# Performance work log

Hardware: AMD Instinct MI355X
Metric: run time of the kernel (lower is better)

## Reference

```python
import jax, jax.numpy as jnp
import numpy as np

IB = 8      # input/hidden activation bits
ABMVM = 8   # gate activation bits after MVM
ABNM = 8    # near-memory compute bits
NL = 0.05   # analog noise level
CY_DIV = 2.0
CY_SCALE = 2.0


def quant_pass(x, wb, sign):
    # Faithful port of QuantFunc.forward: clip/clamp then fake-quant (round to grid).
    if wb is None or wb == 0:
        return x
    if sign:
        delta = 0.0 if wb == 1 else 1.0 / (2.0 ** (wb - 1))
        x = jnp.clip(x, -1.0 + delta, 1.0 - delta)
    else:
        x = jnp.clip(x, 0.0, 1.0)
    if wb == 1:
        return jnp.sign(x)
    scale = 2.0 ** (wb - 1) if sign else 2.0 ** wb
    return jnp.round(x * scale) / scale


def setup_inputs() -> dict:
    key = jax.random.key(0)
    ks = jax.random.split(key, 7)
    B, I, H = 4096, 1024, 1024
    return {
        "input": jax.random.normal(ks[0], (B, I), jnp.float32),
        "hx": jax.random.normal(ks[1], (B, H), jnp.float32),
        "cx": jax.random.normal(ks[2], (B, H), jnp.float32),
        "weight_ih": jax.random.normal(ks[3], (4 * H, I), jnp.float32) * 0.1,
        "weight_hh": jax.random.normal(ks[4], (4 * H, H), jnp.float32) * 0.1,
        "bias_ih": jax.random.normal(ks[5], (4 * H,), jnp.float32) * 0.1,
        "bias_hh": jax.random.normal(ks[6], (4 * H,), jnp.float32) * 0.1,
        "train": 0,
    }


def reference(input, hx, cx, weight_ih, weight_hh, bias_ih, bias_hh, train):
    # Per-call Gaussian noise (simulated analog hardware); fixed key for reproducibility.
    nk = jax.random.split(jax.random.key(42), 4)
    noise_w_ih = jax.random.normal(nk[0], weight_ih.T.shape, weight_ih.dtype) * weight_ih.max() * NL
    noise_w_hh = jax.random.normal(nk[1], weight_hh.T.shape, weight_hh.dtype) * weight_hh.max() * NL
    noise_b_ih = jax.random.normal(nk[2], bias_ih.shape, bias_ih.dtype) * bias_ih.max() * NL
    noise_b_hh = jax.random.normal(nk[3], bias_hh.shape, bias_hh.dtype) * bias_hh.max() * NL

    # gates: [B, 4H]
    gates = (quant_pass(input, IB, True) @ (weight_ih.T + noise_w_ih) + bias_ih + noise_b_ih
             + quant_pass(hx, IB, True) @ (weight_hh.T + noise_w_hh) + bias_hh + noise_b_hh)

    ingate, forgetgate, cellgate, outgate = jnp.split(gates, 4, axis=1)
    ingate = quant_pass(jax.nn.sigmoid(ingate), ABMVM, False)
    forgetgate = quant_pass(jax.nn.sigmoid(forgetgate), ABMVM, False)
    cellgate = quant_pass(jnp.tanh(cellgate), ABMVM, True)
    outgate = quant_pass(jax.nn.sigmoid(outgate), ABMVM, False)

    cy = quant_pass((quant_pass(forgetgate * cx, ABNM, True)
                     + quant_pass(ingate * cellgate, ABNM, True)) / CY_DIV, ABNM, True)
    hy = quant_pass(outgate * quant_pass(jnp.tanh(cy * CY_SCALE), ABNM, True), ABNM, True)
    return (hy, cy)
```

## Files before the change

kernel.cpp:

```cpp
#include <hip/hip_runtime.h>
#include <hip/hip_bf16.h>
#include <stdint.h>
#include <stddef.h>


#define PART 1

typedef __attribute__((ext_vector_type(8))) short bf16x8;
typedef __attribute__((ext_vector_type(4))) float f32x4;

#define BATCH 4096

#define WS_A_OFF    ((size_t)0)
#define WS_B_OFF    ((size_t)16 << 20)
#define WS_BIAS_OFF ((size_t)48 << 20)
#define WS_MAX_OFF  (WS_BIAS_OFF + 16384)

__host__ __device__ inline void tf2x32(uint32_t k0, uint32_t k1,
                                       uint32_t x0, uint32_t x1,
                                       uint32_t &o0, uint32_t &o1)
{
  const uint32_t k2 = k0 ^ k1 ^ 0x1BD11BDAu;
#define TFR(r) { x0 += x1; x1 = (x1 << (r)) | (x1 >> (32 - (r))); x1 ^= x0; }
  x0 += k0; x1 += k1;
  TFR(13) TFR(15) TFR(26) TFR(6)
  x0 += k1; x1 += k2 + 1u;
  TFR(17) TFR(29) TFR(16) TFR(24)
  x0 += k2; x1 += k0 + 2u;
  TFR(13) TFR(15) TFR(26) TFR(6)
  x0 += k0; x1 += k1 + 3u;
  TFR(17) TFR(29) TFR(16) TFR(24)
  x0 += k1; x1 += k2 + 4u;
  TFR(13) TFR(15) TFR(26) TFR(6)
  x0 += k2; x1 += k0 + 5u;
#undef TFR
  o0 = x0; o1 = x1;
}

__device__ inline uint32_t jax_bits32(uint32_t k0, uint32_t k1, uint32_t i, uint32_t size)
{
#if PART
  uint32_t a, b;
  tf2x32(k0, k1, 0u, i, a, b);
  return a ^ b;
#else
  uint32_t half = size >> 1, a, b;
  if (i < half) { tf2x32(k0, k1, i, i + half, a, b); return a; }
  tf2x32(k0, k1, i - half, i, a, b); return b;
#endif
}

__device__ inline float bits_to_normal(uint32_t bits)
{
  float f = __uint_as_float((bits >> 9) | 0x3F800000u) - 1.0f;
  const float lo = -0x1.fffffep-1f;
  float u = fmaxf(lo, f * 2.0f + lo);
  float w = -log1pf(-u * u);
  float p;
  if (w < 5.0f) {
    w -= 2.5f;
    p = 2.81022636e-08f;
    p = fmaf(p, w, 3.43273939e-07f);
    p = fmaf(p, w, -3.5233877e-06f);
    p = fmaf(p, w, -4.39150654e-06f);
    p = fmaf(p, w, 0.00021858087f);
    p = fmaf(p, w, -0.00125372503f);
    p = fmaf(p, w, -0.00417768164f);
    p = fmaf(p, w, 0.246640727f);
    p = fmaf(p, w, 1.50140941f);
  } else {
    w = sqrtf(w) - 3.0f;
    p = -0.000200214257f;
    p = fmaf(p, w, 0.000100950558f);
    p = fmaf(p, w, 0.00134934322f);
    p = fmaf(p, w, -0.00367342844f);
    p = fmaf(p, w, 0.00573950773f);
    p = fmaf(p, w, -0.0076224613f);
    p = fmaf(p, w, 0.00943887047f);
    p = fmaf(p, w, 1.00167406f);
    p = fmaf(p, w, 2.83297682f);
  }
  return 0x1.6a09e6p+0f * (p * u);
}

__device__ inline float quantS8(float x)
{
  x = fminf(fmaxf(x, -0.9921875f), 0.9921875f);
  return rintf(x * 128.0f) * 0.0078125f;
}
__device__ inline float quantU8(float x)
{
  x = fminf(fmaxf(x, 0.0f), 1.0f);
  return rintf(x * 256.0f) * 0.00390625f;
}
__device__ inline float sigmoid_xla(float x) { return 0.5f + 0.5f * tanhf(0.5f * x); }

__device__ inline unsigned short f2bf(float x)
{
  uint32_t b = __float_as_uint(x);
  return (unsigned short)((b + 0x7FFFu + ((b >> 16) & 1u)) >> 16);
}
__device__ inline float bf2f(unsigned short u) { return __uint_as_float(((uint32_t)u) << 16); }

__device__ inline float dec_max(uint32_t u)
{
  uint32_t bits = (u & 0x80000000u) ? (u ^ 0x80000000u) : ~u;
  return __uint_as_float(bits);
}

__global__ void init_max(uint32_t* mx)
{
  if (threadIdx.x < 4) mx[threadIdx.x] = 0u;
}

__global__ void kmax(const float4* __restrict__ a, int n4, uint32_t* __restrict__ out)
{
  float m = -3.4e38f;
  for (int i = blockIdx.x * blockDim.x + threadIdx.x; i < n4; i += gridDim.x * blockDim.x) {
    float4 v = a[i];
    m = fmaxf(fmaxf(m, fmaxf(v.x, v.y)), fmaxf(v.z, v.w));
  }
  for (int off = 32; off; off >>= 1) m = fmaxf(m, __shfl_down(m, off, 64));
  __shared__ float sm[4];
  if ((threadIdx.x & 63) == 0) sm[threadIdx.x >> 6] = m;
  __syncthreads();
  if (threadIdx.x == 0) {
    float bm = sm[0];
    for (int w = 1; w < (int)(blockDim.x >> 6); ++w) bm = fmaxf(bm, sm[w]);
    uint32_t bits = __float_as_uint(bm);
    uint32_t enc = (bits & 0x80000000u) ? ~bits : (bits | 0x80000000u);
    atomicMax(out, enc);
  }
}

__global__ void build_A(const float4* __restrict__ in, const float4* __restrict__ hx,
                        unsigned short* __restrict__ A)
{
  int t = blockIdx.x * 256 + threadIdx.x;
  int b = t >> 9;
  int kq = t & 511;
  float4 v = (kq < 256) ? in[b * 256 + kq] : hx[b * 256 + (kq - 256)];
  unsigned short o[4];
  o[0] = f2bf(quantS8(v.x)); o[1] = f2bf(quantS8(v.y));
  o[2] = f2bf(quantS8(v.z)); o[3] = f2bf(quantS8(v.w));
  *reinterpret_cast<uint64_t*>(A + (size_t)t * 4) = *reinterpret_cast<uint64_t*>(o);
}

__global__ void build_B(const float* __restrict__ wih, const float* __restrict__ whh,
                        unsigned short* __restrict__ B, const uint32_t* __restrict__ mxenc,
                        uint32_t kih0, uint32_t kih1, uint32_t khh0, uint32_t khh1)
{
  uint32_t t = blockIdx.x * 256u + threadIdx.x;
  uint32_t arr = t >> 22;
  uint32_t r = t & 4194303u;
  uint32_t k = r & 1023u;
  uint32_t n = r >> 10;
  const float* w = arr ? whh : wih;
  float mx = dec_max(mxenc[arr]);
  uint32_t key0 = arr ? khh0 : kih0, key1 = arr ? khh1 : kih1;
  uint32_t i = k * 4096u + n;
  float nrm = bits_to_normal(jax_bits32(key0, key1, i, 4194304u));
  float weff = w[(size_t)n * 1024u + k] + (nrm * mx) * 0.05f;
  unsigned short hi = f2bf(weff);
  unsigned short lob = f2bf(weff - bf2f(hi));
  uint32_t np = (n & 1023u) * 4u + (n >> 10);
  size_t base = (size_t)np * 4096u + (arr ? 1024u : 0u) + k;
  B[base] = hi;
  B[base + 2048u] = lob;
}

__global__ void build_bias(const float* __restrict__ bih, const float* __restrict__ bhh,
                           float* __restrict__ biasE, const uint32_t* __restrict__ mxenc,
                           uint32_t kbi0, uint32_t kbi1, uint32_t kbh0, uint32_t kbh1)
{
  uint32_t j = blockIdx.x * 256u + threadIdx.x;
  if (j >= 4096u) return;
  float mi = dec_max(mxenc[2]), mh = dec_max(mxenc[3]);
  float ni = (bits_to_normal(jax_bits32(kbi0, kbi1, j, 4096u)) * mi) * 0.05f;
  float nh = (bits_to_normal(jax_bits32(kbh0, kbh1, j, 4096u)) * mh) * 0.05f;
  biasE[(j & 1023u) * 4u + (j >> 10)] = ((bih[j] + ni) + bhh[j]) + nh;
}

__device__ __forceinline__ void gload_lds16(const void* g, void* l)
{
  __builtin_amdgcn_global_load_lds((__attribute__((address_space(1))) void*)g,
                                   (__attribute__((address_space(3))) void*)l, 16, 0, 0);
}

#define VM4  asm volatile("s_waitcnt vmcnt(4)" ::: "memory")
#define VM0  asm volatile("s_waitcnt vmcnt(0)" ::: "memory")
#define NOVM

#define TILE_ONE(t_, DO_STAGE_, VM_ASM_)                                          \
  {                                                                               \
    const int buf_ = (t_) & 3;                                                    \
    const unsigned char* pa_ = lds + buf_ * 32768 + aoff;                         \
    const unsigned char* pb_ = lds + buf_ * 32768 + boff;                         \
    bf16x8 bfr_[4], afL_[4], afH_[4];                                             \
    _Pragma("unroll") for (int n_ = 0; n_ < 4; ++n_)                              \
      bfr_[n_] = *(const bf16x8*)(pb_ + n_ * 1024);                               \
    _Pragma("unroll") for (int m_ = 0; m_ < 4; ++m_)                              \
      afL_[m_] = *(const bf16x8*)(pa_ + m_ * 1024);                               \
    _Pragma("unroll") for (int m_ = 0; m_ < 4; ++m_)                              \
      afH_[m_] = *(const bf16x8*)(pa_ + (4 + m_) * 1024);                         \
    if (DO_STAGE_) {                                                              \
      const int ts_ = (t_) + 2;                                                   \
      unsigned char* la_ = lds + (ts_ & 3) * 32768;                               \
      const int ka_ = (ts_ * 32) & 2047;                                          \
      const size_t kb_ = (size_t)ts_ * 32;                                        \
      gload_lds16(Ar0 + ka_, la_ + tid * 16);                                     \
      gload_lds16(Ar1 + ka_, la_ + 8192 + tid * 16);                              \
      gload_lds16(Br0 + kb_, la_ + 16384 + tid * 16);                             \
      gload_lds16(Br1 + kb_, la_ + 16384 + 8192 + tid * 16);                      \
    }                                                                             \
    __builtin_amdgcn_s_setprio(1);                                                \
    _Pragma("unroll") for (int m_ = 0; m_ < 4; ++m_)                              \
      _Pragma("unroll") for (int n_ = 0; n_ < 4; ++n_)                            \
        acc[m_][n_] = __builtin_amdgcn_mfma_f32_16x16x32_bf16(afL_[m_], bfr_[n_], \
                                                              acc[m_][n_], 0, 0, 0); \
    _Pragma("unroll") for (int m_ = 0; m_ < 4; ++m_)                              \
      _Pragma("unroll") for (int n_ = 0; n_ < 4; ++n_)                            \
        acc[4 + m_][n_] = __builtin_amdgcn_mfma_f32_16x16x32_bf16(afH_[m_], bfr_[n_], \
                                                              acc[4 + m_][n_], 0, 0, 0); \
    __builtin_amdgcn_s_setprio(0);                                                \
    VM_ASM_;                                                                      \
    __builtin_amdgcn_s_barrier();                                                 \
    __builtin_amdgcn_sched_barrier(0);                                            \
  }

__global__ __launch_bounds__(512, 2) void gemm_gates(
    const unsigned short* __restrict__ A,
    const unsigned short* __restrict__ B,
    const float* __restrict__ bias,
    const float* __restrict__ cx,
    float* __restrict__ hy,
    float* __restrict__ cy)
{
  extern __shared__ unsigned char lds[];
  const int tid  = threadIdx.x;
  const int lane = tid & 63;
  const int wave = tid >> 6;
  const int wr = wave >> 2;
  const int wc = wave & 3;

  const int bid = blockIdx.x;
  const int wg  = (bid & 7) * 32 + (bid >> 3);
  const int brow = (wg & 15) * 256;
  const int bcol = (wg >> 4) * 256;

  int sr0, sk0, sr1, sk1;
  {
    int c = tid, p = c >> 3, lc = (c & 7) ^ (p & 7);
    sr0 = p * 2 + (lc >> 2); sk0 = (lc & 3) * 8;
    c = tid + 512; p = c >> 3; lc = (c & 7) ^ (p & 7);
    sr1 = p * 2 + (lc >> 2); sk1 = (lc & 3) * 8;
  }
  const unsigned short* Ar0 = A + (size_t)(brow + sr0) * 2048 + sk0;
  const unsigned short* Ar1 = A + (size_t)(brow + sr1) * 2048 + sk1;
  const unsigned short* Br0 = B + (size_t)(bcol + sr0) * 4096 + sk0;
  const unsigned short* Br1 = B + (size_t)(bcol + sr1) * 4096 + sk1;

  const int lrh = (lane & 15) >> 1;
  const int chk = ((((lane & 1) << 2) | (lane >> 4)) ^ lrh);
  const int aoff = wr * 8192 + lrh * 128 + chk * 16;
  const int boff = 16384 + wc * 4096 + lrh * 128 + chk * 16;

  f32x4 acc[8][4] = {};

#pragma unroll
  for (int tt = 0; tt < 2; ++tt) {
    unsigned char* la = lds + tt * 32768;
    const int ka = tt * 32;
    gload_lds16(Ar0 + ka, la + tid * 16);
    gload_lds16(Ar1 + ka, la + 8192 + tid * 16);
    gload_lds16(Br0 + (size_t)(tt * 32), la + 16384 + tid * 16);
    gload_lds16(Br1 + (size_t)(tt * 32), la + 16384 + 8192 + tid * 16);
  }
  VM4;
  __builtin_amdgcn_s_barrier();
  __builtin_amdgcn_sched_barrier(0);

#pragma unroll 1
  for (int t = 0; t < 126; ++t) {
    TILE_ONE(t, 1, VM4);
  }
  TILE_ONE(126, 0, VM0);
  TILE_ONE(127, 0, NOVM);

  float* LT = (float*)lds;
  const int col_local0 = wc * 64 + (lane & 15);
  const int lrow = (lane >> 4) << 2;
  const int h = tid & 63;
  const int hg = (bcol >> 2) + h;

#pragma unroll
  for (int hh = 0; hh < 2; ++hh) {
    __syncthreads();
#pragma unroll
    for (int m = 0; m < 4; ++m) {
#pragma unroll
      for (int n = 0; n < 4; ++n) {
        const int cl = col_local0 + n * 16;
        const float bv = bias[bcol + cl];
        const int lr0 = wr * 64 + m * 16 + lrow;
#pragma unroll
        for (int r = 0; r < 4; ++r)
          LT[(lr0 + r) * 256 + cl] = acc[hh * 4 + m][n][r] + bv;
      }
    }
    __syncthreads();
#pragma unroll
    for (int i = 0; i < 16; ++i) {
      const int lr = (tid >> 6) * 16 + i;
      const int grow = brow + ((lr >> 6) << 7) + hh * 64 + (lr & 63);
      const float4 q = *(const float4*)(LT + lr * 256 + 4 * h);
      const size_t oidx = (size_t)grow * 1024 + hg;
      float ing = quantU8(sigmoid_xla(q.x));
      float fg  = quantU8(sigmoid_xla(q.y));
      float cg  = quantS8(tanhf(q.z));
      float og  = quantU8(sigmoid_xla(q.w));
      float c0  = cx[oidx];
      float cyv = quantS8((quantS8(fg * c0) + quantS8(ing * cg)) * 0.5f);
      float hyv = quantS8(og * quantS8(tanhf(cyv * 2.0f)));
      hy[oidx] = hyv;
      cy[oidx] = cyv;
    }
  }
}

extern "C" void kernel_launch(void* const* d_in, const int* in_sizes, int n_in,
                              void* d_out, int out_size, void* d_ws, size_t ws_size,
                              hipStream_t stream)
{
  const float* input = (const float*)d_in[0];
  const float* hx    = (const float*)d_in[1];
  const float* cx    = (const float*)d_in[2];
  const float* wih   = (const float*)d_in[3];
  const float* whh   = (const float*)d_in[4];
  const float* bih   = (const float*)d_in[5];
  const float* bhh   = (const float*)d_in[6];
  (void)in_sizes; (void)n_in; (void)ws_size;

  uint8_t* ws = (uint8_t*)d_ws;
  unsigned short* A   = (unsigned short*)(ws + WS_A_OFF);
  unsigned short* B   = (unsigned short*)(ws + WS_B_OFF);
  float* biasE        = (float*)(ws + WS_BIAS_OFF);
  uint32_t* mx        = (uint32_t*)(ws + WS_MAX_OFF);

  uint32_t nk[4][2];
#if PART
  for (int i = 0; i < 4; ++i) tf2x32(0u, 42u, 0u, (uint32_t)i, nk[i][0], nk[i][1]);
#else
  {
    uint32_t w0[4], w1[4];
    for (int i = 0; i < 4; ++i) tf2x32(0u, 42u, (uint32_t)i, (uint32_t)(i + 4), w0[i], w1[i]);
    uint32_t out8[8] = {w0[0], w0[1], w0[2], w0[3], w1[0], w1[1], w1[2], w1[3]};
    for (int i = 0; i < 4; ++i) { nk[i][0] = out8[2 * i]; nk[i][1] = out8[2 * i + 1]; }
  }
#endif

  init_max<<<1, 64, 0, stream>>>(mx);
  kmax<<<1024, 256, 0, stream>>>((const float4*)wih, 1048576, mx + 0);
  kmax<<<1024, 256, 0, stream>>>((const float4*)whh, 1048576, mx + 1);
  kmax<<<4, 256, 0, stream>>>((const float4*)bih, 1024, mx + 2);
  kmax<<<4, 256, 0, stream>>>((const float4*)bhh, 1024, mx + 3);

  build_A<<<8192, 256, 0, stream>>>((const float4*)input, (const float4*)hx, A);
  build_B<<<32768, 256, 0, stream>>>(wih, whh, B, mx, nk[0][0], nk[0][1], nk[1][0], nk[1][1]);
  build_bias<<<16, 256, 0, stream>>>(bih, bhh, biasE, mx, nk[2][0], nk[2][1], nk[3][0], nk[3][1]);

  float* hy = (float*)d_out;
  float* cyp = hy + (size_t)BATCH * 1024;

  (void)hipFuncSetAttribute((const void*)gemm_gates,
                            hipFuncAttributeMaxDynamicSharedMemorySize, 131072);
  gemm_gates<<<dim3(256), dim3(512), 131072, stream>>>(A, B, biasE, cx, hy, cyp);
}
```

Baseline: 230.6 us.

## Fuse prep kernels, split-bf16 B with double buffering, pad epilogue LDS tile

Merges the four max-reduction launches into one kernel and the A/B/bias build kernels into one, cutting launch count. The GEMM main loop is restructured to stage both hi and lo bf16 halves of B in a double-buffered 48KB LDS layout. Each K-tile is now 64 tiles with extra barriers between MFMA phases, and it waits with vmcnt(0) each iteration instead of the old 4-deep ring. The epilogue LDS transpose stride is padded to 272 floats to reduce bank conflicts. The shallower prefetch and added barriers risk exposing memory latency, and the LDS footprint rises.

```diff
diff --git a/kernel.cpp b/kernel.cpp
--- a/kernel.cpp
+++ b/kernel.cpp
@@ -113,11 +113,20 @@
   if (threadIdx.x < 4) mx[threadIdx.x] = 0u;
 }
 
-__global__ void kmax(const float4* __restrict__ a, int n4, uint32_t* __restrict__ out)
-{
+__global__ void kmax_all(const float4* __restrict__ wih, const float4* __restrict__ whh,
+                         const float4* __restrict__ bih, const float4* __restrict__ bhh,
+                         uint32_t* __restrict__ mx)
+{
+  const int blk = blockIdx.x;
+  const float4* src; int n4, bl, nb; uint32_t* out;
+  if (blk < 1024)      { src = wih; n4 = 1048576; bl = blk;        nb = 1024; out = mx + 0; }
+  else if (blk < 2048) { src = whh; n4 = 1048576; bl = blk - 1024; nb = 1024; out = mx + 1; }
+  else if (blk < 2052) { src = bih; n4 = 1024;    bl = blk - 2048; nb = 4;    out = mx + 2; }
+  else                 { src = bhh; n4 = 1024;    bl = blk - 2052; nb = 4;    out = mx + 3; }
+
   float m = -3.4e38f;
-  for (int i = blockIdx.x * blockDim.x + threadIdx.x; i < n4; i += gridDim.x * blockDim.x) {
-    float4 v = a[i];
+  for (int i = bl * 256 + threadIdx.x; i < n4; i += nb * 256) {
+    float4 v = src[i];
     m = fmaxf(fmaxf(m, fmaxf(v.x, v.y)), fmaxf(v.z, v.w));
   }
   for (int off = 32; off; off >>= 1) m = fmaxf(m, __shfl_down(m, off, 64));
@@ -125,60 +134,56 @@
   if ((threadIdx.x & 63) == 0) sm[threadIdx.x >> 6] = m;
   __syncthreads();
   if (threadIdx.x == 0) {
-    float bm = sm[0];
-    for (int w = 1; w < (int)(blockDim.x >> 6); ++w) bm = fmaxf(bm, sm[w]);
+    float bm = fmaxf(fmaxf(sm[0], sm[1]), fmaxf(sm[2], sm[3]));
     uint32_t bits = __float_as_uint(bm);
     uint32_t enc = (bits & 0x80000000u) ? ~bits : (bits | 0x80000000u);
     atomicMax(out, enc);
   }
 }
 
-__global__ void build_A(const float4* __restrict__ in, const float4* __restrict__ hx,
-                        unsigned short* __restrict__ A)
-{
-  int t = blockIdx.x * 256 + threadIdx.x;
-  int b = t >> 9;
-  int kq = t & 511;
-  float4 v = (kq < 256) ? in[b * 256 + kq] : hx[b * 256 + (kq - 256)];
-  unsigned short o[4];
-  o[0] = f2bf(quantS8(v.x)); o[1] = f2bf(quantS8(v.y));
-  o[2] = f2bf(quantS8(v.z)); o[3] = f2bf(quantS8(v.w));
-  *reinterpret_cast<uint64_t*>(A + (size_t)t * 4) = *reinterpret_cast<uint64_t*>(o);
-}
-
-__global__ void build_B(const float* __restrict__ wih, const float* __restrict__ whh,
-                        unsigned short* __restrict__ B, const uint32_t* __restrict__ mxenc,
-                        uint32_t kih0, uint32_t kih1, uint32_t khh0, uint32_t khh1)
-{
-  uint32_t t = blockIdx.x * 256u + threadIdx.x;
-  uint32_t arr = t >> 22;
-  uint32_t r = t & 4194303u;
-  uint32_t k = r & 1023u;
-  uint32_t n = r >> 10;
-  const float* w = arr ? whh : wih;
-  float mx = dec_max(mxenc[arr]);
-  uint32_t key0 = arr ? khh0 : kih0, key1 = arr ? khh1 : kih1;
-  uint32_t i = k * 4096u + n;
-  float nrm = bits_to_normal(jax_bits32(key0, key1, i, 4194304u));
-  float weff = w[(size_t)n * 1024u + k] + (nrm * mx) * 0.05f;
-  unsigned short hi = f2bf(weff);
-  unsigned short lob = f2bf(weff - bf2f(hi));
-  uint32_t np = (n & 1023u) * 4u + (n >> 10);
-  size_t base = (size_t)np * 4096u + (arr ? 1024u : 0u) + k;
-  B[base] = hi;
-  B[base + 2048u] = lob;
-}
-
-__global__ void build_bias(const float* __restrict__ bih, const float* __restrict__ bhh,
-                           float* __restrict__ biasE, const uint32_t* __restrict__ mxenc,
-                           uint32_t kbi0, uint32_t kbi1, uint32_t kbh0, uint32_t kbh1)
-{
-  uint32_t j = blockIdx.x * 256u + threadIdx.x;
-  if (j >= 4096u) return;
-  float mi = dec_max(mxenc[2]), mh = dec_max(mxenc[3]);
-  float ni = (bits_to_normal(jax_bits32(kbi0, kbi1, j, 4096u)) * mi) * 0.05f;
-  float nh = (bits_to_normal(jax_bits32(kbh0, kbh1, j, 4096u)) * mh) * 0.05f;
-  biasE[(j & 1023u) * 4u + (j >> 10)] = ((bih[j] + ni) + bhh[j]) + nh;
+__global__ void build_all(const float* __restrict__ wih, const float* __restrict__ whh,
+                          const float4* __restrict__ in, const float4* __restrict__ hxp,
+                          const float* __restrict__ bih, const float* __restrict__ bhh,
+                          unsigned short* __restrict__ A, unsigned short* __restrict__ B,
+                          float* __restrict__ biasE, const uint32_t* __restrict__ mxenc,
+                          uint32_t kih0, uint32_t kih1, uint32_t khh0, uint32_t khh1,
+                          uint32_t kbi0, uint32_t kbi1, uint32_t kbh0, uint32_t kbh1)
+{
+  const uint32_t blk = blockIdx.x;
+  if (blk < 32768u) {
+    uint32_t t = blk * 256u + threadIdx.x;
+    uint32_t arr = t >> 22;
+    uint32_t r = t & 4194303u;
+    uint32_t k = r & 1023u;
+    uint32_t n = r >> 10;
+    const float* w = arr ? whh : wih;
+    float mx = dec_max(mxenc[arr]);
+    uint32_t key0 = arr ? khh0 : kih0, key1 = arr ? khh1 : kih1;
+    uint32_t i = k * 4096u + n;
+    float nrm = bits_to_normal(jax_bits32(key0, key1, i, 4194304u));
+    float weff = w[(size_t)n * 1024u + k] + (nrm * mx) * 0.05f;
+    unsigned short hi = f2bf(weff);
+    unsigned short lob = f2bf(weff - bf2f(hi));
+    uint32_t np = (n & 1023u) * 4u + (n >> 10);
+    size_t base = (size_t)np * 4096u + (arr ? 1024u : 0u) + k;
+    B[base] = hi;
+    B[base + 2048u] = lob;
+  } else if (blk < 40960u) {
+    int t = (int)(blk - 32768u) * 256 + threadIdx.x;
+    int b = t >> 9;
+    int kq = t & 511;
+    float4 v = (kq < 256) ? in[b * 256 + kq] : hxp[b * 256 + (kq - 256)];
+    unsigned short o[4];
+    o[0] = f2bf(quantS8(v.x)); o[1] = f2bf(quantS8(v.y));
+    o[2] = f2bf(quantS8(v.z)); o[3] = f2bf(quantS8(v.w));
+    *reinterpret_cast<uint64_t*>(A + (size_t)t * 4) = *reinterpret_cast<uint64_t*>(o);
+  } else {
+    uint32_t j = (blk - 40960u) * 256u + threadIdx.x;
+    float mi = dec_max(mxenc[2]), mh = dec_max(mxenc[3]);
+    float ni = (bits_to_normal(jax_bits32(kbi0, kbi1, j, 4096u)) * mi) * 0.05f;
+    float nh = (bits_to_normal(jax_bits32(kbh0, kbh1, j, 4096u)) * mh) * 0.05f;
+    biasE[(j & 1023u) * 4u + (j >> 10)] = ((bih[j] + ni) + bhh[j]) + nh;
+  }
 }
 
 __device__ __forceinline__ void gload_lds16(const void* g, void* l)
@@ -187,46 +192,74 @@
                                    (__attribute__((address_space(3))) void*)l, 16, 0, 0);
 }
 
-#define VM4  asm volatile("s_waitcnt vmcnt(4)" ::: "memory")
 #define VM0  asm volatile("s_waitcnt vmcnt(0)" ::: "memory")
 #define NOVM
+#define SBAR __builtin_amdgcn_s_barrier()
+#define SCB  __builtin_amdgcn_sched_barrier(0)
+
+#define BUFSZ 49152
 
 #define TILE_ONE(t_, DO_STAGE_, VM_ASM_)                                          \
   {                                                                               \
-    const int buf_ = (t_) & 3;                                                    \
-    const unsigned char* pa_ = lds + buf_ * 32768 + aoff;                         \
-    const unsigned char* pb_ = lds + buf_ * 32768 + boff;                         \
-    bf16x8 bfr_[4], afL_[4], afH_[4];                                             \
+    const int buf_ = (t_) & 1;                                                    \
+    const unsigned char* pa_  = lds + buf_ * BUFSZ + aoff;                        \
+    const unsigned char* pbh_ = lds + buf_ * BUFSZ + 16384 + boffU;               \
+    const unsigned char* pbl_ = lds + buf_ * BUFSZ + 32768 + boffU;               \
+    bf16x8 bh_[4], bl_[4], afL_[4], afH_[4];                                      \
+                 \
     _Pragma("unroll") for (int n_ = 0; n_ < 4; ++n_)                              \
-      bfr_[n_] = *(const bf16x8*)(pb_ + n_ * 1024);                               \
+      bh_[n_] = *(const bf16x8*)(pbh_ + n_ * 1024);                               \
     _Pragma("unroll") for (int m_ = 0; m_ < 4; ++m_)                              \
       afL_[m_] = *(const bf16x8*)(pa_ + m_ * 1024);                               \
-    _Pragma("unroll") for (int m_ = 0; m_ < 4; ++m_)                              \
-      afH_[m_] = *(const bf16x8*)(pa_ + (4 + m_) * 1024);                         \
     if (DO_STAGE_) {                                                              \
-      const int ts_ = (t_) + 2;                                                   \
-      unsigned char* la_ = lds + (ts_ & 3) * 32768;                               \
-      const int ka_ = (ts_ * 32) & 2047;                                          \
-      const size_t kb_ = (size_t)ts_ * 32;                                        \
+      const int ts_ = (t_) + 1;                                                   \
+      unsigned char* la_ = lds + (ts_ & 1) * BUFSZ;                               \
+      const int ka_ = ts_ * 32;                                                   \
       gload_lds16(Ar0 + ka_, la_ + tid * 16);                                     \
       gload_lds16(Ar1 + ka_, la_ + 8192 + tid * 16);                              \
-      gload_lds16(Br0 + kb_, la_ + 16384 + tid * 16);                             \
-      gload_lds16(Br1 + kb_, la_ + 16384 + 8192 + tid * 16);                      \
+      gload_lds16(Br0 + ka_, la_ + 16384 + tid * 16);                             \
+      gload_lds16(Br1 + ka_, la_ + 16384 + 8192 + tid * 16);                      \
+      gload_lds16(Br0 + 2048 + ka_, la_ + 32768 + tid * 16);                      \
+      gload_lds16(Br1 + 2048 + ka_, la_ + 32768 + 8192 + tid * 16);               \
     }                                                                             \
+    SBAR; SCB;                                                                    \
     __builtin_amdgcn_s_setprio(1);                                                \
     _Pragma("unroll") for (int m_ = 0; m_ < 4; ++m_)                              \
       _Pragma("unroll") for (int n_ = 0; n_ < 4; ++n_)                            \
-        acc[m_][n_] = __builtin_amdgcn_mfma_f32_16x16x32_bf16(afL_[m_], bfr_[n_], \
+        acc[m_][n_] = __builtin_amdgcn_mfma_f32_16x16x32_bf16(afL_[m_], bh_[n_],  \
                                                               acc[m_][n_], 0, 0, 0); \
+    __builtin_amdgcn_s_setprio(0);                                                \
+    SBAR; SCB;                                                                    \
+                                                       \
+    _Pragma("unroll") for (int m_ = 0; m_ < 4; ++m_)                              \
+      afH_[m_] = *(const bf16x8*)(pa_ + (4 + m_) * 1024);                         \
+    SBAR; SCB;                                                                    \
+    __builtin_amdgcn_s_setprio(1);                                                \
     _Pragma("unroll") for (int m_ = 0; m_ < 4; ++m_)                              \
       _Pragma("unroll") for (int n_ = 0; n_ < 4; ++n_)                            \
-        acc[4 + m_][n_] = __builtin_amdgcn_mfma_f32_16x16x32_bf16(afH_[m_], bfr_[n_], \
+        acc[4 + m_][n_] = __builtin_amdgcn_mfma_f32_16x16x32_bf16(afH_[m_], bh_[n_], \
+                                                              acc[4 + m_][n_], 0, 0, 0); \
+    __builtin_amdgcn_s_setprio(0);                                                \
+    SBAR; SCB;                                                                    \
+                         \
+    _Pragma("unroll") for (int n_ = 0; n_ < 4; ++n_)                              \
+      bl_[n_] = *(const bf16x8*)(pbl_ + n_ * 1024);                               \
+    SBAR; SCB;                                                                    \
+    __builtin_amdgcn_s_setprio(1);                                                \
+    _Pragma("unroll") for (int m_ = 0; m_ < 4; ++m_)                              \
+      _Pragma("unroll") for (int n_ = 0; n_ < 4; ++n_)                            \
+        acc[m_][n_] = __builtin_amdgcn_mfma_f32_16x16x32_bf16(afL_[m_], bl_[n_],  \
+                                                              acc[m_][n_], 0, 0, 0); \
+    _Pragma("unroll") for (int m_ = 0; m_ < 4; ++m_)                              \
+      _Pragma("unroll") for (int n_ = 0; n_ < 4; ++n_)                            \
+        acc[4 + m_][n_] = __builtin_amdgcn_mfma_f32_16x16x32_bf16(afH_[m_], bl_[n_], \
                                                               acc[4 + m_][n_], 0, 0, 0); \
     __builtin_amdgcn_s_setprio(0);                                                \
     VM_ASM_;                                                                      \
-    __builtin_amdgcn_s_barrier();                                                 \
-    __builtin_amdgcn_sched_barrier(0);                                            \
-  }
+    SBAR; SCB;                                                                    \
+  }
+
+#define LTS 272
 
 __global__ __launch_bounds__(512, 2) void gemm_gates(
     const unsigned short* __restrict__ A,
@@ -262,30 +295,25 @@
 
   const int lrh = (lane & 15) >> 1;
   const int chk = ((((lane & 1) << 2) | (lane >> 4)) ^ lrh);
-  const int aoff = wr * 8192 + lrh * 128 + chk * 16;
-  const int boff = 16384 + wc * 4096 + lrh * 128 + chk * 16;
+  const int aoff  = wr * 8192 + lrh * 128 + chk * 16;
+  const int boffU = wc * 4096 + lrh * 128 + chk * 16;
 
   f32x4 acc[8][4] = {};
 
-#pragma unroll
-  for (int tt = 0; tt < 2; ++tt) {
-    unsigned char* la = lds + tt * 32768;
-    const int ka = tt * 32;
-    gload_lds16(Ar0 + ka, la + tid * 16);
-    gload_lds16(Ar1 + ka, la + 8192 + tid * 16);
-    gload_lds16(Br0 + (size_t)(tt * 32), la + 16384 + tid * 16);
-    gload_lds16(Br1 + (size_t)(tt * 32), la + 16384 + 8192 + tid * 16);
-  }
-  VM4;
-  __builtin_amdgcn_s_barrier();
-  __builtin_amdgcn_sched_barrier(0);
+  gload_lds16(Ar0, lds + tid * 16);
+  gload_lds16(Ar1, lds + 8192 + tid * 16);
+  gload_lds16(Br0, lds + 16384 + tid * 16);
+  gload_lds16(Br1, lds + 16384 + 8192 + tid * 16);
+  gload_lds16(Br0 + 2048, lds + 32768 + tid * 16);
+  gload_lds16(Br1 + 2048, lds + 32768 + 8192 + tid * 16);
+  VM0;
+  SBAR; SCB;
 
 #pragma unroll 1
-  for (int t = 0; t < 126; ++t) {
-    TILE_ONE(t, 1, VM4);
-  }
-  TILE_ONE(126, 0, VM0);
-  TILE_ONE(127, 0, NOVM);
+  for (int t = 0; t < 63; ++t) {
+    TILE_ONE(t, 1, VM0);
+  }
+  TILE_ONE(63, 0, NOVM);
 
   float* LT = (float*)lds;
   const int col_local0 = wc * 64 + (lane & 15);
@@ -305,7 +333,7 @@
         const int lr0 = wr * 64 + m * 16 + lrow;
 #pragma unroll
         for (int r = 0; r < 4; ++r)
-          LT[(lr0 + r) * 256 + cl] = acc[hh * 4 + m][n][r] + bv;
+          LT[(lr0 + r) * LTS + cl] = acc[hh * 4 + m][n][r] + bv;
       }
     }
     __syncthreads();
@@ -313,7 +341,7 @@
     for (int i = 0; i < 16; ++i) {
       const int lr = (tid >> 6) * 16 + i;
       const int grow = brow + ((lr >> 6) << 7) + hh * 64 + (lr & 63);
-      const float4 q = *(const float4*)(LT + lr * 256 + 4 * h);
+      const float4 q = *(const float4*)(LT + lr * LTS + 4 * h);
       const size_t oidx = (size_t)grow * 1024 + hg;
       float ing = quantU8(sigmoid_xla(q.x));
       float fg  = quantU8(sigmoid_xla(q.y));
@@ -360,19 +388,17 @@
 #endif
 
   init_max<<<1, 64, 0, stream>>>(mx);
-  kmax<<<1024, 256, 0, stream>>>((const float4*)wih, 1048576, mx + 0);
-  kmax<<<1024, 256, 0, stream>>>((const float4*)whh, 1048576, mx + 1);
-  kmax<<<4, 256, 0, stream>>>((const float4*)bih, 1024, mx + 2);
-  kmax<<<4, 256, 0, stream>>>((const float4*)bhh, 1024, mx + 3);
-
-  build_A<<<8192, 256, 0, stream>>>((const float4*)input, (const float4*)hx, A);
-  build_B<<<32768, 256, 0, stream>>>(wih, whh, B, mx, nk[0][0], nk[0][1], nk[1][0], nk[1][1]);
-  build_bias<<<16, 256, 0, stream>>>(bih, bhh, biasE, mx, nk[2][0], nk[2][1], nk[3][0], nk[3][1]);
+  kmax_all<<<2056, 256, 0, stream>>>((const float4*)wih, (const float4*)whh,
+                                     (const float4*)bih, (const float4*)bhh, mx);
+  build_all<<<40976, 256, 0, stream>>>(wih, whh, (const float4*)input, (const float4*)hx,
+                                       bih, bhh, A, B, biasE, mx,
+                                       nk[0][0], nk[0][1], nk[1][0], nk[1][1],
+                                       nk[2][0], nk[2][1], nk[3][0], nk[3][1]);
 
   float* hy = (float*)d_out;
   float* cyp = hy + (size_t)BATCH * 1024;
 
   (void)hipFuncSetAttribute((const void*)gemm_gates,
-                            hipFuncAttributeMaxDynamicSharedMemorySize, 131072);
-  gemm_gates<<<dim3(256), dim3(512), 131072, stream>>>(A, B, biasE, cx, hy, cyp);
-}
+                            hipFuncAttributeMaxDynamicSharedMemorySize, 139264);
+  gemm_gates<<<dim3(256), dim3(512), 139264, stream>>>(A, B, biasE, cx, hy, cyp);
+}
```

After: 214.9 us. 6.8% less time.
